# Kernel optimization log

Hardware: AMD Instinct MI355X
Metric: run time of the kernel (lower is better)

## Reference

```python
import jax, jax.numpy as jnp
import numpy as np

B, N, D, H, K = 8, 10000, 128, 4, 256
DH = D // H
M = N // 2


def make_pe(n, d):
    pos = jnp.arange(n, dtype=jnp.float32)[:, None]
    div = jnp.exp(jnp.arange(0, d, 2, dtype=jnp.float32) * (-jnp.log(10000.0) / d))
    ang = pos * div  # [n, d/2]
    pe = jnp.zeros((n, d), dtype=jnp.float32)
    pe = pe.at[:, 0::2].set(jnp.sin(ang))
    pe = pe.at[:, 1::2].set(jnp.cos(ang))
    return pe


def layernorm(z, g, b, eps=1e-5):
    mu = jnp.mean(z, -1, keepdims=True)
    var = jnp.var(z, -1, keepdims=True)
    return (z - mu) / jnp.sqrt(var + eps) * g + b


def setup_inputs():
    key = jax.random.key(0)
    ks = jax.random.split(key, 12)
    def rn(k, shape, scale):
        return jax.random.normal(k, shape, dtype=jnp.float32) * scale
    return {
        "x": rn(ks[0], (B, N), 1.0),
        "emb_w": rn(ks[1], (D, 1), 0.5),
        "emb_b": rn(ks[2], (D,), 0.02),
        "ln1_g": jnp.ones((D,), jnp.float32),
        "ln1_b": jnp.zeros((D,), jnp.float32),
        "wq": rn(ks[3], (D, D), D ** -0.5),
        "wk": rn(ks[4], (D, D), D ** -0.5),
        "wv": rn(ks[5], (D, D), D ** -0.5),
        "proj_k": rn(ks[6], (N, K), N ** -0.5),
        "proj_v": rn(ks[7], (N, K), N ** -0.5),
        "wo": rn(ks[8], (D, D), D ** -0.5),
        "wo_b": jnp.zeros((D,), jnp.float32),
        "ln2_g": jnp.ones((D,), jnp.float32),
        "ln2_b": jnp.zeros((D,), jnp.float32),
        "w1": rn(ks[9], (4 * D, D), D ** -0.5),
        "b1": jnp.zeros((4 * D,), jnp.float32),
        "w2": rn(ks[10], (D, 4 * D), (4 * D) ** -0.5),
        "b2": jnp.zeros((D,), jnp.float32),
        "fc_w": rn(ks[11], (M, N), N ** -0.5),
        "fc_b": jnp.zeros((M,), jnp.float32),
    }


def reference(x, emb_w, emb_b, ln1_g, ln1_b, wq, wk, wv, proj_k, proj_v, wo, wo_b,
              ln2_g, ln2_b, w1, b1, w2, b2, fc_w, fc_b):
    b, n = x.shape
    # Linear embedding of scalar per position: [B,N] -> [B,N,D]
    xe = x[..., None] @ emb_w.T + emb_b
    xe = xe + make_pe(n, D)
    # --- Linformer self-attention block (pre-norm + residual) ---
    hn = layernorm(xe, ln1_g, ln1_b)
    q = hn @ wq.T                                        # [B,N,D]
    k = jnp.einsum('bnd,nk->bkd', hn @ wk.T, proj_k)     # low-rank keys   [B,K,D]
    v = jnp.einsum('bnd,nk->bkd', hn @ wv.T, proj_v)     # low-rank values [B,K,D]
    q = q.reshape(b, n, H, DH).transpose(0, 2, 1, 3)     # [B,H,N,DH]
    k = k.reshape(b, K, H, DH).transpose(0, 2, 1, 3)     # [B,H,K,DH]
    v = v.reshape(b, K, H, DH).transpose(0, 2, 1, 3)
    attn = jax.nn.softmax(jnp.einsum('bhnd,bhkd->bhnk', q, k) * (DH ** -0.5), axis=-1)
    out = jnp.einsum('bhnk,bhkd->bhnd', attn, v).transpose(0, 2, 1, 3).reshape(b, n, D)
    xe = xe + out @ wo.T + wo_b
    # --- FeedForward block (pre-norm + residual, exact GELU) ---
    hn = layernorm(xe, ln2_g, ln2_b)
    xe = xe + (jax.nn.gelu(hn @ w1.T + b1, approximate=False) @ w2.T + b2)
    # fc over seq dim (Linear(N, N//2) applied to [B,D,N]) then sum-pool over D
    y = jnp.einsum('bnd,mn->bdm', xe, fc_w) + fc_b       # [B,D,M]
    return jnp.sum(y, axis=1)                            # [B,M]
```

## Files before the change

### kernel.cpp

```cpp
#include <hip/hip_runtime.h>

constexpr int B_ = 8, N_ = 10000, D_ = 128, H_ = 4, K_ = 256, M_ = 5000, DFF_ = 512;
constexpr int NPAD = 10240;

typedef __attribute__((ext_vector_type(8))) short bf16x8;
typedef __attribute__((ext_vector_type(4))) float f32x4;

__device__ __forceinline__ float bf2f(unsigned short u) {
    unsigned x = ((unsigned)u) << 16; float f; __builtin_memcpy(&f, &x, 4); return f;
}
__device__ __forceinline__ unsigned short f2bf(float f) {
    unsigned x; __builtin_memcpy(&x, &f, 4);
    x = (x + 0x7fffu + ((x >> 16) & 1u)) >> 16;
    return (unsigned short)x;
}
__device__ __forceinline__ unsigned pack2(float a, float b) {
    return (unsigned)f2bf(a) | ((unsigned)f2bf(b) << 16);
}
__device__ __forceinline__ float gelu_exact(float v) {
    return 0.5f * v * (1.0f + erff(v * 0.70710678118654752f));
}

__global__ __launch_bounds__(256) void cvt_w_k(
    const float* __restrict__ s0, const float* __restrict__ s1, const float* __restrict__ s2,
    const float* __restrict__ s3, const float* __restrict__ s4, const float* __restrict__ s5,
    unsigned short* __restrict__ d0, unsigned short* __restrict__ d1, unsigned short* __restrict__ d2,
    unsigned short* __restrict__ d3, unsigned short* __restrict__ d4, unsigned short* __restrict__ d5)
{
    const float* s; unsigned short* d; int sz;
    switch (blockIdx.y) {
        case 0: s = s0; d = d0; sz = 16384; break;
        case 1: s = s1; d = d1; sz = 16384; break;
        case 2: s = s2; d = d2; sz = 16384; break;
        case 3: s = s3; d = d3; sz = 16384; break;
        case 4: s = s4; d = d4; sz = 65536; break;
        default: s = s5; d = d5; sz = 65536; break;
    }
    const int idx = (blockIdx.x * 256 + threadIdx.x) * 8;
    if (idx >= sz) return;
    float4 a = *(const float4*)(s + idx);
    float4 b = *(const float4*)(s + idx + 4);
    uint4 p;
    p.x = pack2(a.x, a.y); p.y = pack2(a.z, a.w);
    p.z = pack2(b.x, b.y); p.w = pack2(b.z, b.w);
    *(uint4*)(d + idx) = p;
}

__global__ __launch_bounds__(256) void ptt_k(
    const float* __restrict__ pK, const float* __restrict__ pV, unsigned short* __restrict__ Pt)
{
    __shared__ __align__(16) char lds[16384];
    const int t = threadIdx.x;
    const int n0 = blockIdx.x * 64, k0 = blockIdx.y * 128, which = blockIdx.z;
    const float* P = which ? pV : pK;
    {
        const int nl = t >> 2, cc = t & 3;
        const int n = n0 + nl;
        uint4 v[4] = {};
        if (n < N_) {
            const float4* src = (const float4*)(P + (size_t)n * K_ + k0 + cc * 32);
            #pragma unroll
            for (int j = 0; j < 4; ++j) {
                float4 a = src[2 * j], b = src[2 * j + 1];
                uint4 p; p.x = pack2(a.x, a.y); p.y = pack2(a.z, a.w);
                p.z = pack2(b.x, b.y); p.w = pack2(b.z, b.w);
                v[j] = p;
            }
        }
        #pragma unroll
        for (int j = 0; j < 4; ++j) {
            int ch = (cc * 4 + j) ^ (nl & 15);
            *(uint4*)(lds + nl * 256 + ch * 16) = v[j];
        }
    }
    __syncthreads();
    {
        const int eb = t >> 3, nb = t & 7;
        unsigned short r0_[8], r1_[8], r2_[8], r3_[8];
        #pragma unroll
        for (int i = 0; i < 8; ++i) {
            int n = nb * 8 + i;
            int byte_ = n * 256 + (((eb >> 1) ^ (n & 15)) << 4) + ((eb & 1) << 3);
            uint2 dv = *(const uint2*)(lds + byte_);
            r0_[i] = (unsigned short)(dv.x & 0xffff); r1_[i] = (unsigned short)(dv.x >> 16);
            r2_[i] = (unsigned short)(dv.y & 0xffff); r3_[i] = (unsigned short)(dv.y >> 16);
        }
        size_t dbase = ((size_t)which * 256 + k0 + eb * 4) * NPAD + n0 + nb * 8;
        *(uint4*)&Pt[dbase]            = *(uint4*)r0_;
        *(uint4*)&Pt[dbase + NPAD]     = *(uint4*)r1_;
        *(uint4*)&Pt[dbase + 2 * NPAD] = *(uint4*)r2_;
        *(uint4*)&Pt[dbase + 3 * NPAD] = *(uint4*)r3_;
    }
}

__global__ __launch_bounds__(256) void hnt_k(
    const unsigned short* __restrict__ hn, unsigned short* __restrict__ hnT)
{
    __shared__ __align__(16) char lds[16384];
    const int t = threadIdx.x;
    const int n0 = blockIdx.x * 64, b = blockIdx.z;
    {
        const int nl = t >> 2, cc = t & 3;
        const int n = n0 + nl;
        uint4 v[4] = {};
        if (n < N_) {
            const uint4* src = (const uint4*)(hn + ((size_t)(b * N_ + n)) * D_ + cc * 32);
            #pragma unroll
            for (int j = 0; j < 4; ++j) v[j] = src[j];
        }
        #pragma unroll
        for (int j = 0; j < 4; ++j) {
            int ch = (cc * 4 + j) ^ (nl & 15);
            *(uint4*)(lds + nl * 256 + ch * 16) = v[j];
        }
    }
    __syncthreads();
    {
        const int eb = t >> 3, nb = t & 7;
        unsigned short r0_[8], r1_[8], r2_[8], r3_[8];
        #pragma unroll
        for (int i = 0; i < 8; ++i) {
            int n = nb * 8 + i;
            int byte_ = n * 256 + (((eb >> 1) ^ (n & 15)) << 4) + ((eb & 1) << 3);
            uint2 dv = *(const uint2*)(lds + byte_);
            r0_[i] = (unsigned short)(dv.x & 0xffff); r1_[i] = (unsigned short)(dv.x >> 16);
            r2_[i] = (unsigned short)(dv.y & 0xffff); r3_[i] = (unsigned short)(dv.y >> 16);
        }
        size_t dbase = ((size_t)b * 128 + eb * 4) * NPAD + n0 + nb * 8;
        *(uint4*)&hnT[dbase]            = *(uint4*)r0_;
        *(uint4*)&hnT[dbase + NPAD]     = *(uint4*)r1_;
        *(uint4*)&hnT[dbase + 2 * NPAD] = *(uint4*)r2_;
        *(uint4*)&hnT[dbase + 3 * NPAD] = *(uint4*)r3_;
    }
}

__global__ __launch_bounds__(256) void embed_ln_k(
    const float* __restrict__ x, const float* __restrict__ ew, const float* __restrict__ eb,
    const float* __restrict__ g, const float* __restrict__ bb,
    unsigned short* __restrict__ xeb, unsigned short* __restrict__ hnb)
{
    const int r = blockIdx.x * 4 + (threadIdx.x >> 6);
    const int lane = threadIdx.x & 63;
    const int n = r % N_;
    const float xv = x[r];
    const float ang = (float)n * expf((float)lane * -0.14391156829962788f);
    float sv, cv; sincosf(ang, &sv, &cv);
    const int d0 = 2 * lane;
    float e0 = xv * ew[d0]     + eb[d0]     + sv;
    float e1 = xv * ew[d0 + 1] + eb[d0 + 1] + cv;
    float sum = e0 + e1, sq = e0 * e0 + e1 * e1;
    #pragma unroll
    for (int off = 32; off; off >>= 1) { sum += __shfl_xor(sum, off); sq += __shfl_xor(sq, off); }
    const float mu = sum * (1.f / 128.f);
    const float var = sq * (1.f / 128.f) - mu * mu;
    const float rs = rsqrtf(var + 1e-5f);
    const size_t base = (size_t)r * D_ + d0;
    *(unsigned*)&xeb[base] = pack2(e0, e1);
    *(unsigned*)&hnb[base] = pack2((e0 - mu) * rs * g[d0] + bb[d0],
                                   (e1 - mu) * rs * g[d0 + 1] + bb[d0 + 1]);
}

enum { M_Q = 0, M_PROJ = 1, M_SMALL = 2, M_WO = 3, M_W1 = 4, M_W2 = 5 };

template<int MODE>
__global__ __launch_bounds__(256) void mgemm_k(
    const unsigned short* __restrict__ Abase, const unsigned short* __restrict__ Wbase,
    const unsigned short* __restrict__ Walt,
    const float* __restrict__ bias, float* __restrict__ Cf, unsigned short* __restrict__ Cb,
    const unsigned short* __restrict__ xebr, unsigned short* __restrict__ xebw,
    const float* __restrict__ lng, const float* __restrict__ lnb, float* __restrict__ st)
{
    constexpr int NSTEP = (MODE == M_PROJ) ? 40 : (MODE == M_W2 ? 16 : 4);
    constexpr int SA = (MODE == M_PROJ) ? NPAD : (MODE == M_W2 ? 512 : 128);
    constexpr int SB = SA;
    constexpr int NCTOT = (MODE == M_W1) ? 512 : 128;
    constexpr bool GELU = (MODE == M_W1);
    constexpr bool FUSED = (MODE == M_WO || MODE == M_W2);

    __shared__ __align__(16) char lds[16384];

    const int t = threadIdx.x;
    const int bx = blockIdx.x, by = blockIdx.y, bz = blockIdx.z;

    const unsigned short* Ag; const unsigned short* Wg; size_t cbase;
    if (MODE == M_PROJ) {
        const int b = (bz >> 3) & 7, chunk = bz & 7, which = bz >> 6;
        Ag = Abase + (size_t)which * 256 * NPAD + (size_t)bx * 128 * NPAD + chunk * 1280;
        Wg = Wbase + (size_t)b * 128 * NPAD + chunk * 1280;
        cbase = (size_t)bz * 32768 + (size_t)bx * 16384;
    } else if (MODE == M_SMALL) {
        Ag = Abase + (size_t)bz * 2048 * 128 + (size_t)bx * 128 * 128;
        Wg = bz ? Walt : Wbase;
        cbase = (size_t)bz * 262144 + (size_t)bx * 16384;
    } else {
        Ag = Abase + (size_t)bx * 128 * SA;
        Wg = Wbase + (size_t)by * 128 * SB;
        cbase = (size_t)bx * 128 * NCTOT + (size_t)by * 128;
    }

    const int srow = t >> 1, hib = 2 * (t & 1);
    const unsigned short* aptr = Ag + (size_t)srow * SA + hib * 8;
    const unsigned short* wptr = Wg + (size_t)srow * SB + hib * 8;
    const int swz = (srow >> 1) & 3;
    char* la0 = lds + srow * 64 + ((hib ^ swz) << 4);
    char* la1 = lds + srow * 64 + (((hib + 1) ^ swz) << 4);
    char* lw0 = la0 + 8192;
    char* lw1 = la1 + 8192;

    const int w = t >> 6, l = t & 63;
    const int g = l >> 4;
    const int wrow = (w & 1) * 64, wcol = (w >> 1) * 64;
    int offA[4], offW[4];
    #pragma unroll
    for (int mi = 0; mi < 4; ++mi) {
        int ra = wrow + mi * 16 + (l & 15);
        offA[mi] = ra * 64 + (((l >> 4) ^ ((ra >> 1) & 3)) << 4);
        int rw = wcol + mi * 16 + (l & 15);
        offW[mi] = 8192 + rw * 64 + (((l >> 4) ^ ((rw >> 1) & 3)) << 4);
    }

    f32x4 acc[4][4] = {};

    for (int s = 0; s < NSTEP; ++s) {
        uint4 va0 = *(const uint4*)(aptr);
        uint4 va1 = *(const uint4*)(aptr + 8);
        uint4 vw0 = *(const uint4*)(wptr);
        uint4 vw1 = *(const uint4*)(wptr + 8);
        aptr += 32; wptr += 32;
        __syncthreads();
        *(uint4*)la0 = va0; *(uint4*)la1 = va1;
        *(uint4*)lw0 = vw0; *(uint4*)lw1 = vw1;
        __syncthreads();
        bf16x8 af[4], bfr[4];
        #pragma unroll
        for (int mi = 0; mi < 4; ++mi) {
            af[mi] = *(const bf16x8*)(lds + offA[mi]);
            bfr[mi] = *(const bf16x8*)(lds + offW[mi]);
        }
        #pragma unroll
        for (int mi = 0; mi < 4; ++mi)
            #pragma unroll
            for (int ni = 0; ni < 4; ++ni)
                acc[mi][ni] = __builtin_amdgcn_mfma_f32_16x16x32_bf16(af[mi], bfr[ni], acc[mi][ni], 0, 0, 0);
    }

    const int lrb = wrow + (g << 2);
    const int lcb = wcol + (l & 15);

    if (FUSED) {
        float rsum[4][4], rsq[4][4];
        #pragma unroll
        for (int mi = 0; mi < 4; ++mi)
            #pragma unroll
            for (int r = 0; r < 4; ++r) { rsum[mi][r] = 0.f; rsq[mi][r] = 0.f; }
        #pragma unroll
        for (int mi = 0; mi < 4; ++mi)
            #pragma unroll
            for (int ni = 0; ni < 4; ++ni) {
                const int lc = lcb + ni * 16;
                #pragma unroll
                for (int r = 0; r < 4; ++r) {
                    const int lr = lrb + mi * 16 + r;
                    const size_t ci = cbase + (size_t)lr * 128 + lc;
                    float v = acc[mi][ni][r] + bias[lc] + bf2f(xebr[ci]);
                    acc[mi][ni][r] = v;
                    rsum[mi][r] += v;
                    if (MODE == M_WO) rsq[mi][r] += v * v;
                }
            }
        #pragma unroll
        for (int mi = 0; mi < 4; ++mi)
            #pragma unroll
            for (int r = 0; r < 4; ++r) {
                float s_ = rsum[mi][r], q_ = rsq[mi][r];
                #pragma unroll
                for (int off = 1; off < 16; off <<= 1) {
                    s_ += __shfl_xor(s_, off);
                    if (MODE == M_WO) q_ += __shfl_xor(q_, off);
                }
                rsum[mi][r] = s_; rsq[mi][r] = q_;
            }
        __syncthreads();
        float2* red = (float2*)lds;
        if ((l & 15) == 0) {
            #pragma unroll
            for (int mi = 0; mi < 4; ++mi)
                #pragma unroll
                for (int r = 0; r < 4; ++r) {
                    const int lr = lrb + mi * 16 + r;
                    float2 e; e.x = rsum[mi][r]; e.y = rsq[mi][r];
                    red[(w >> 1) * 128 + lr] = e;
                }
        }
        __syncthreads();
        if (MODE == M_WO) {
            #pragma unroll
            for (int mi = 0; mi < 4; ++mi)
                #pragma unroll
                for (int r = 0; r < 4; ++r) {
                    const int lr = lrb + mi * 16 + r;
                    const float2 e0 = red[lr], e1 = red[128 + lr];
                    const float mu = (e0.x + e1.x) * (1.f / 128.f);
                    const float var = (e0.y + e1.y) * (1.f / 128.f) - mu * mu;
                    const float rstd = rsqrtf(var + 1e-5f);
                    #pragma unroll
                    for (int ni = 0; ni < 4; ++ni) {
                        const int lc = lcb + ni * 16;
                        const size_t ci = cbase + (size_t)lr * 128 + lc;
                        const float xv = acc[mi][ni][r];
                        xebw[ci] = f2bf(xv);
                        Cb[ci] = f2bf((xv - mu) * rstd * lng[lc] + lnb[lc]);
                    }
                }
        } else {
            if ((l & 15) == 0 && (w >> 1) == 0) {
                #pragma unroll
                for (int mi = 0; mi < 4; ++mi)
                    #pragma unroll
                    for (int r = 0; r < 4; ++r) {
                        const int lr = lrb + mi * 16 + r;
                        const float total = red[lr].x + red[128 + lr].x;
                        const int grow = bx * 128 + lr;
                        const int bidx = grow / N_;
                        const int n = grow - bidx * N_;
                        st[(size_t)n * 8 + bidx] = total;
                    }
            }
        }
        return;
    }

    constexpr bool HASBIAS = (MODE == M_W1);
    constexpr bool OBF = (MODE == M_Q || MODE == M_W1 || MODE == M_SMALL);
    #pragma unroll
    for (int mi = 0; mi < 4; ++mi) {
        #pragma unroll
        for (int ni = 0; ni < 4; ++ni) {
            const int lc = lcb + ni * 16;
            #pragma unroll
            for (int r = 0; r < 4; ++r) {
                const int lr = lrb + mi * 16 + r;
                float v = acc[mi][ni][r];
                if (HASBIAS) v += bias[by * 128 + lc];
                if (GELU) v = gelu_exact(v);
                const size_t ci = cbase + (size_t)lr * NCTOT + lc;
                if (OBF) Cb[ci] = f2bf(v); else Cf[ci] = v;
            }
        }
    }
}

__global__ __launch_bounds__(256) void reduce_k(
    const float* __restrict__ partials, unsigned short* __restrict__ lowKV)
{
    const int gid = blockIdx.x * 256 + threadIdx.x;
    const int wb = gid >> 15, r = gid & 32767;
    const float* p = partials + (size_t)wb * 8 * 32768 + r;
    float s = 0.f;
    #pragma unroll
    for (int c = 0; c < 8; ++c) s += p[c * 32768];
    lowKV[gid] = f2bf(s);
}

__global__ __launch_bounds__(256) void attn_mfma_k(
    const unsigned short* __restrict__ q, const unsigned short* __restrict__ kv,
    unsigned short* __restrict__ outp)
{
    __shared__ __align__(16) char lds[65536];
    const int t = threadIdx.x;
    const int w = t >> 6, l = t & 63;
    const int g = l >> 4, ql = l & 15;
    const int h = blockIdx.y, b = blockIdx.z;
    const int q0 = blockIdx.x * 256;
    const float SC = 0.17677669529663687f;

    #pragma unroll
    for (int i = 0; i < 4; ++i) {
        const int r = (t >> 2) + 64 * i;
        const uint4 v = *(const uint4*)(kv + ((size_t)(b * 256 + r) * 128 + h * 32) + (t & 3) * 8);
        *(uint4*)(lds + r * 64 + (((t & 3) * 16) ^ ((r & 3) << 4))) = v;
    }
    {
        const int kp = t & 127, dhalf = t >> 7;
        const unsigned short* vsrc = kv + 262144 + ((size_t)(b * 256 + 2 * kp) * 128 + h * 32 + 16 * dhalf);
        uint4 a0 = *(const uint4*)(vsrc);
        uint4 a1 = *(const uint4*)(vsrc + 8);
        uint4 c0 = *(const uint4*)(vsrc + 128);
        uint4 c1 = *(const uint4*)(vsrc + 136);
        const unsigned short* pa0 = (const unsigned short*)&a0;
        const unsigned short* pa1 = (const unsigned short*)&a1;
        const unsigned short* pc0 = (const unsigned short*)&c0;
        const unsigned short* pc1 = (const unsigned short*)&c1;
        #pragma unroll
        for (int j = 0; j < 8; ++j) {
            const int row = 16 * dhalf + j;
            unsigned u = (unsigned)pa0[j] | ((unsigned)pc0[j] << 16);
            *(unsigned*)(lds + 16384 + row * 512 + ((4 * kp) ^ ((row & 7) << 4))) = u;
        }
        #pragma unroll
        for (int j = 0; j < 8; ++j) {
            const int row = 16 * dhalf + 8 + j;
            unsigned u = (unsigned)pa1[j] | ((unsigned)pc1[j] << 16);
            *(unsigned*)(lds + 16384 + row * 512 + ((4 * kp) ^ ((row & 7) << 4))) = u;
        }
    }
    bf16x8 qfr[4];
    #pragma unroll
    for (int qf = 0; qf < 4; ++qf) {
        int n = q0 + w * 64 + qf * 16 + ql;
        if (n >= N_) n = N_ - 1;
        qfr[qf] = *(const bf16x8*)(q + ((size_t)(b * N_ + n) * 128 + h * 32 + g * 8));
    }
    __syncthreads();

    char* Pw = lds + 32768 + w * 8192;
    f32x4 oacc[2][4] = {};
    float m_run[4], l_run[4];
    #pragma unroll
    for (int qf = 0; qf < 4; ++qf) { m_run[qf] = -1e30f; l_run[qf] = 0.f; }

    for (int kt = 0; kt < 4; ++kt) {
        const int kb = kt * 64;
        bf16x8 kfr[4];
        #pragma unroll
        for (int kf = 0; kf < 4; ++kf) {
            const int r = kb + kf * 16 + ql;
            kfr[kf] = *(const bf16x8*)(lds + r * 64 + ((g * 16) ^ ((r & 3) << 4)));
        }
        f32x4 s_[4][4];
        #pragma unroll
        for (int kf = 0; kf < 4; ++kf)
            #pragma unroll
            for (int qf = 0; qf < 4; ++qf) {
                f32x4 z = {0.f, 0.f, 0.f, 0.f};
                s_[kf][qf] = __builtin_amdgcn_mfma_f32_16x16x32_bf16(kfr[kf], qfr[qf], z, 0, 0, 0);
            }
        #pragma unroll
        for (int qf = 0; qf < 4; ++qf) {
            float mx = -1e30f;
            #pragma unroll
            for (int kf = 0; kf < 4; ++kf)
                #pragma unroll
                for (int r = 0; r < 4; ++r) mx = fmaxf(mx, s_[kf][qf][r]);
            mx = fmaxf(mx, __shfl_xor(mx, 16));
            mx = fmaxf(mx, __shfl_xor(mx, 32));
            mx *= SC;
            if (mx > m_run[qf]) {
                const float corr = __expf(m_run[qf] - mx);
                l_run[qf] *= corr;
                #pragma unroll
                for (int df = 0; df < 2; ++df) {
                    oacc[df][qf][0] *= corr; oacc[df][qf][1] *= corr;
                    oacc[df][qf][2] *= corr; oacc[df][qf][3] *= corr;
                }
                m_run[qf] = mx;
            }
            float p_[4][4]; float ssum = 0.f;
            #pragma unroll
            for (int kf = 0; kf < 4; ++kf)
                #pragma unroll
                for (int r = 0; r < 4; ++r) {
                    const float pv = __expf(s_[kf][qf][r] * SC - m_run[qf]);
                    p_[kf][r] = pv; ssum += pv;
                }
            ssum += __shfl_xor(ssum, 16);
            ssum += __shfl_xor(ssum, 32);
            l_run[qf] += ssum;
            const int qrow = qf * 16 + ql;
            #pragma unroll
            for (int kf = 0; kf < 4; ++kf) {
                uint2 pk;
                pk.x = pack2(p_[kf][0], p_[kf][1]);
                pk.y = pack2(p_[kf][2], p_[kf][3]);
                *(uint2*)(Pw + qrow * 128 + ((kf * 32 + g * 8) ^ ((qrow & 7) << 4))) = pk;
            }
        }
        asm volatile("s_waitcnt lgkmcnt(0)" ::: "memory");
        __builtin_amdgcn_sched_barrier(0);
        #pragma unroll
        for (int ks = 0; ks < 2; ++ks) {
            bf16x8 vt_[2];
            #pragma unroll
            for (int df = 0; df < 2; ++df) {
                const int row = df * 16 + ql;
                vt_[df] = *(const bf16x8*)(lds + 16384 + row * 512 +
                           ((kb * 2 + ks * 64 + g * 16) ^ ((row & 7) << 4)));
            }
            #pragma unroll
            for (int qf = 0; qf < 4; ++qf) {
                const int qrow = qf * 16 + ql;
                bf16x8 pf = *(const bf16x8*)(Pw + qrow * 128 + ((ks * 64 + g * 16) ^ ((qrow & 7) << 4)));
                #pragma unroll
                for (int df = 0; df < 2; ++df)
                    oacc[df][qf] = __builtin_amdgcn_mfma_f32_16x16x32_bf16(vt_[df], pf, oacc[df][qf], 0, 0, 0);
            }
        }
        asm volatile("s_waitcnt lgkmcnt(0)" ::: "memory");
        __builtin_amdgcn_sched_barrier(0);
    }

    float inv_[4];
    #pragma unroll
    for (int qf = 0; qf < 4; ++qf) inv_[qf] = 1.f / l_run[qf];
    #pragma unroll
    for (int qf = 0; qf < 4; ++qf) {
        const int qrow = qf * 16 + ql;
        #pragma unroll
        for (int df = 0; df < 2; ++df) {
            const unsigned lo = pack2(oacc[df][qf][0] * inv_[qf], oacc[df][qf][1] * inv_[qf]);
            const unsigned hi = pack2(oacc[df][qf][2] * inv_[qf], oacc[df][qf][3] * inv_[qf]);
            *(unsigned*)(Pw + qrow * 64 + ((df * 32 + g * 8) ^ ((qrow & 3) << 4))) = lo;
            *(unsigned*)(Pw + qrow * 64 + ((df * 32 + g * 8 + 4) ^ ((qrow & 3) << 4))) = hi;
        }
    }
    asm volatile("s_waitcnt lgkmcnt(0)" ::: "memory");
    __builtin_amdgcn_sched_barrier(0);
    #pragma unroll
    for (int pp = 0; pp < 4; ++pp) {
        const int qrow = pp * 16 + (l >> 2), c = l & 3;
        const uint4 v = *(const uint4*)(Pw + qrow * 64 + ((c * 16) ^ ((qrow & 3) << 4)));
        const int n = q0 + w * 64 + qrow;
        if (n < N_)
            *(uint4*)(outp + ((size_t)(b * N_ + n) * 128 + h * 32 + c * 8)) = v;
    }
}

__global__ __launch_bounds__(256) void fc_k(
    const float* __restrict__ st, const float* __restrict__ fcw, const float* __restrict__ fcb,
    float* __restrict__ out)
{
    __shared__ float wred[4][4][8];
    const int t = threadIdx.x;
    const int m0 = blockIdx.x * 4;
    float acc[4][8] = {};
    for (int n = t; n < N_; n += 256) {
        const float4 sa = *(const float4*)&st[(size_t)n * 8];
        const float4 sb = *(const float4*)&st[(size_t)n * 8 + 4];
        #pragma unroll
        for (int mm = 0; mm < 4; ++mm) {
            const float w = fcw[(size_t)(m0 + mm) * N_ + n];
            acc[mm][0] = fmaf(w, sa.x, acc[mm][0]); acc[mm][1] = fmaf(w, sa.y, acc[mm][1]);
            acc[mm][2] = fmaf(w, sa.z, acc[mm][2]); acc[mm][3] = fmaf(w, sa.w, acc[mm][3]);
            acc[mm][4] = fmaf(w, sb.x, acc[mm][4]); acc[mm][5] = fmaf(w, sb.y, acc[mm][5]);
            acc[mm][6] = fmaf(w, sb.z, acc[mm][6]); acc[mm][7] = fmaf(w, sb.w, acc[mm][7]);
        }
    }
    #pragma unroll
    for (int mm = 0; mm < 4; ++mm)
        #pragma unroll
        for (int bb = 0; bb < 8; ++bb) {
            float v = acc[mm][bb];
            #pragma unroll
            for (int off = 32; off; off >>= 1) v += __shfl_xor(v, off);
            acc[mm][bb] = v;
        }
    const int lane = t & 63, wv_ = t >> 6;
    if (lane == 0)
        #pragma unroll
        for (int mm = 0; mm < 4; ++mm)
            #pragma unroll
            for (int bb = 0; bb < 8; ++bb) wred[wv_][mm][bb] = acc[mm][bb];
    __syncthreads();
    if (t < 32) {
        const int mm = t >> 3, bb = t & 7;
        float v = wred[0][mm][bb] + wred[1][mm][bb] + wred[2][mm][bb] + wred[3][mm][bb];
        out[(size_t)bb * M_ + m0 + mm] = v + 128.f * fcb[m0 + mm];
    }
}

extern "C" void kernel_launch(void* const* d_in, const int* in_sizes, int n_in,
                              void* d_out, int out_size, void* d_ws, size_t ws_size,
                              hipStream_t stream)
{
    const float* x      = (const float*)d_in[0];
    const float* emb_w  = (const float*)d_in[1];
    const float* emb_b  = (const float*)d_in[2];
    const float* ln1_g  = (const float*)d_in[3];
    const float* ln1_b  = (const float*)d_in[4];
    const float* wq     = (const float*)d_in[5];
    const float* wk     = (const float*)d_in[6];
    const float* wv     = (const float*)d_in[7];
    const float* projk  = (const float*)d_in[8];
    const float* projv  = (const float*)d_in[9];
    const float* wo     = (const float*)d_in[10];
    const float* wo_b   = (const float*)d_in[11];
    const float* ln2_g  = (const float*)d_in[12];
    const float* ln2_b  = (const float*)d_in[13];
    const float* w1     = (const float*)d_in[14];
    const float* b1     = (const float*)d_in[15];
    const float* w2     = (const float*)d_in[16];
    const float* b2     = (const float*)d_in[17];
    const float* fcw    = (const float*)d_in[18];
    const float* fcb    = (const float*)d_in[19];
    float* out = (float*)d_out;

    char* W = (char*)d_ws;
    unsigned short* xeb      = (unsigned short*)W;
    unsigned short* hnb      = (unsigned short*)(W + 40960000);
    char*           region   = W + 61440000;
    unsigned short* qb       = (unsigned short*)region;
    unsigned short* hnT      = (unsigned short*)(region + 20480000);
    unsigned short* Pt       = (unsigned short*)(region + 41451520);
    float*          partials = (float*)(region + 51937280);
    unsigned short* hid      = (unsigned short*)region;
    unsigned short* lowKV    = (unsigned short*)(W + 146931712);
    unsigned short* klowb    = (unsigned short*)(W + 147980288);
    unsigned short* wqb      = (unsigned short*)(W + 150077440);
    unsigned short* wkb      = wqb + 16384;
    unsigned short* wvb      = wkb + 16384;
    unsigned short* wob      = wvb + 16384;
    unsigned short* w1b      = wob + 16384;
    unsigned short* w2b      = w1b + 65536;
    float*          st       = (float*)(W + 150470656);

    const size_t BN = (size_t)B_ * N_;

    cvt_w_k<<<dim3(32, 6), 256, 0, stream>>>(wq, wk, wv, wo, w1, w2, wqb, wkb, wvb, wob, w1b, w2b);
    ptt_k<<<dim3(160, 2, 2), 256, 0, stream>>>(projk, projv, Pt);
    embed_ln_k<<<BN / 4, 256, 0, stream>>>(x, emb_w, emb_b, ln1_g, ln1_b, xeb, hnb);
    hnt_k<<<dim3(160, 1, 8), 256, 0, stream>>>(hnb, hnT);
    mgemm_k<M_Q><<<dim3(625, 1, 1), 256, 0, stream>>>(hnb, wqb, nullptr, nullptr, nullptr, qb,
                                                      nullptr, nullptr, nullptr, nullptr, nullptr);
    mgemm_k<M_PROJ><<<dim3(2, 1, 128), 256, 0, stream>>>(Pt, hnT, nullptr, nullptr, partials, nullptr,
                                                         nullptr, nullptr, nullptr, nullptr, nullptr);
    reduce_k<<<2048, 256, 0, stream>>>(partials, lowKV);
    mgemm_k<M_SMALL><<<dim3(16, 1, 2), 256, 0, stream>>>(lowKV, wkb, wvb, nullptr, nullptr, klowb,
                                                         nullptr, nullptr, nullptr, nullptr, nullptr);
    attn_mfma_k<<<dim3(40, H_, B_), 256, 0, stream>>>(qb, klowb, hnb);
    mgemm_k<M_WO><<<dim3(625, 1, 1), 256, 0, stream>>>(hnb, wob, nullptr, wo_b, nullptr, hnb,
                                                       xeb, xeb, ln2_g, ln2_b, nullptr);
    mgemm_k<M_W1><<<dim3(625, 4, 1), 256, 0, stream>>>(hnb, w1b, nullptr, b1, nullptr, hid,
                                                       nullptr, nullptr, nullptr, nullptr, nullptr);
    mgemm_k<M_W2><<<dim3(625, 1, 1), 256, 0, stream>>>(hid, w2b, nullptr, b2, nullptr, nullptr,
                                                       xeb, nullptr, nullptr, nullptr, st);
    fc_k<<<M_ / 4, 256, 0, stream>>>(st, fcw, fcb, out);
}
```

Baseline: 328.8 us.

## Fuse FFN into one kernel, merge prep kernels, fold reduction into GEMM

Replaces the separate W1 (with GELU) and W2 GEMM launches with a single fused FFN kernel. The 512-wide hidden activation now stays in shared memory per 64-row tile instead of going through a global buffer. The two prep kernels are merged into one launch, and the partial-sum reduction for the low-rank K/V is folded into the small GEMM's A-load. The fc kernel is also vectorized to load four positions at a time. The FFN kernel reads weight fragments directly from global memory without LDS staging, and its smaller tiles may cost some MFMA efficiency.

```diff
diff --git a/kernel.cpp b/kernel.cpp
--- a/kernel.cpp
+++ b/kernel.cpp
@@ -21,37 +21,42 @@
     return 0.5f * v * (1.0f + erff(v * 0.70710678118654752f));
 }
 
-__global__ __launch_bounds__(256) void cvt_w_k(
-    const float* __restrict__ s0, const float* __restrict__ s1, const float* __restrict__ s2,
-    const float* __restrict__ s3, const float* __restrict__ s4, const float* __restrict__ s5,
-    unsigned short* __restrict__ d0, unsigned short* __restrict__ d1, unsigned short* __restrict__ d2,
-    unsigned short* __restrict__ d3, unsigned short* __restrict__ d4, unsigned short* __restrict__ d5)
-{
-    const float* s; unsigned short* d; int sz;
-    switch (blockIdx.y) {
-        case 0: s = s0; d = d0; sz = 16384; break;
-        case 1: s = s1; d = d1; sz = 16384; break;
-        case 2: s = s2; d = d2; sz = 16384; break;
-        case 3: s = s3; d = d3; sz = 16384; break;
-        case 4: s = s4; d = d4; sz = 65536; break;
-        default: s = s5; d = d5; sz = 65536; break;
-    }
-    const int idx = (blockIdx.x * 256 + threadIdx.x) * 8;
-    if (idx >= sz) return;
-    float4 a = *(const float4*)(s + idx);
-    float4 b = *(const float4*)(s + idx + 4);
-    uint4 p;
-    p.x = pack2(a.x, a.y); p.y = pack2(a.z, a.w);
-    p.z = pack2(b.x, b.y); p.w = pack2(b.z, b.w);
-    *(uint4*)(d + idx) = p;
-}
-
-__global__ __launch_bounds__(256) void ptt_k(
+__global__ __launch_bounds__(256) void prep_k(
+    const float* __restrict__ wq, const float* __restrict__ wk, const float* __restrict__ wv,
+    const float* __restrict__ wo, const float* __restrict__ w1, const float* __restrict__ w2,
+    unsigned short* __restrict__ wqb, unsigned short* __restrict__ wkb, unsigned short* __restrict__ wvb,
+    unsigned short* __restrict__ wob, unsigned short* __restrict__ w1b, unsigned short* __restrict__ w2b,
     const float* __restrict__ pK, const float* __restrict__ pV, unsigned short* __restrict__ Pt)
 {
     __shared__ __align__(16) char lds[16384];
     const int t = threadIdx.x;
-    const int n0 = blockIdx.x * 64, k0 = blockIdx.y * 128, which = blockIdx.z;
+    const int flat = blockIdx.x;
+
+    if (flat < 192) {
+        const int by = flat / 32, bx = flat % 32;
+        const float* s; unsigned short* d; int sz;
+        switch (by) {
+            case 0: s = wq; d = wqb; sz = 16384; break;
+            case 1: s = wk; d = wkb; sz = 16384; break;
+            case 2: s = wv; d = wvb; sz = 16384; break;
+            case 3: s = wo; d = wob; sz = 16384; break;
+            case 4: s = w1; d = w1b; sz = 65536; break;
+            default: s = w2; d = w2b; sz = 65536; break;
+        }
+        const int idx = (bx * 256 + t) * 8;
+        if (idx >= sz) return;
+        float4 a = *(const float4*)(s + idx);
+        float4 b = *(const float4*)(s + idx + 4);
+        uint4 p;
+        p.x = pack2(a.x, a.y); p.y = pack2(a.z, a.w);
+        p.z = pack2(b.x, b.y); p.w = pack2(b.z, b.w);
+        *(uint4*)(d + idx) = p;
+        return;
+    }
+
+    const int f = flat - 192;
+    const int bx = f % 160, rest = f / 160;
+    const int n0 = bx * 64, k0 = (rest & 1) * 128, which = rest >> 1;
     const float* P = which ? pV : pK;
     {
         const int nl = t >> 2, cc = t & 3;
@@ -160,7 +165,7 @@
                                    (e1 - mu) * rs * g[d0 + 1] + bb[d0 + 1]);
 }
 
-enum { M_Q = 0, M_PROJ = 1, M_SMALL = 2, M_WO = 3, M_W1 = 4, M_W2 = 5 };
+enum { M_Q = 0, M_PROJ = 1, M_SMALL = 2, M_WO = 3 };
 
 template<int MODE>
 __global__ __launch_bounds__(256) void mgemm_k(
@@ -168,38 +173,35 @@
     const unsigned short* __restrict__ Walt,
     const float* __restrict__ bias, float* __restrict__ Cf, unsigned short* __restrict__ Cb,
     const unsigned short* __restrict__ xebr, unsigned short* __restrict__ xebw,
-    const float* __restrict__ lng, const float* __restrict__ lnb, float* __restrict__ st)
+    const float* __restrict__ lng, const float* __restrict__ lnb)
 {
-    constexpr int NSTEP = (MODE == M_PROJ) ? 40 : (MODE == M_W2 ? 16 : 4);
-    constexpr int SA = (MODE == M_PROJ) ? NPAD : (MODE == M_W2 ? 512 : 128);
+    constexpr int NSTEP = (MODE == M_PROJ) ? 40 : 4;
+    constexpr int SA = (MODE == M_PROJ) ? NPAD : 128;
     constexpr int SB = SA;
-    constexpr int NCTOT = (MODE == M_W1) ? 512 : 128;
-    constexpr bool GELU = (MODE == M_W1);
-    constexpr bool FUSED = (MODE == M_WO || MODE == M_W2);
+    constexpr bool FUSED = (MODE == M_WO);
 
     __shared__ __align__(16) char lds[16384];
 
     const int t = threadIdx.x;
-    const int bx = blockIdx.x, by = blockIdx.y, bz = blockIdx.z;
-
-    const unsigned short* Ag; const unsigned short* Wg; size_t cbase;
+    const int bx = blockIdx.x, bz = blockIdx.z;
+
+    const unsigned short* Ag = nullptr; const unsigned short* Wg; size_t cbase;
     if (MODE == M_PROJ) {
         const int b = (bz >> 3) & 7, chunk = bz & 7, which = bz >> 6;
         Ag = Abase + (size_t)which * 256 * NPAD + (size_t)bx * 128 * NPAD + chunk * 1280;
         Wg = Wbase + (size_t)b * 128 * NPAD + chunk * 1280;
         cbase = (size_t)bz * 32768 + (size_t)bx * 16384;
     } else if (MODE == M_SMALL) {
-        Ag = Abase + (size_t)bz * 2048 * 128 + (size_t)bx * 128 * 128;
         Wg = bz ? Walt : Wbase;
         cbase = (size_t)bz * 262144 + (size_t)bx * 16384;
     } else {
         Ag = Abase + (size_t)bx * 128 * SA;
-        Wg = Wbase + (size_t)by * 128 * SB;
-        cbase = (size_t)bx * 128 * NCTOT + (size_t)by * 128;
+        Wg = Wbase;
+        cbase = (size_t)bx * 128 * 128;
     }
 
     const int srow = t >> 1, hib = 2 * (t & 1);
-    const unsigned short* aptr = Ag + (size_t)srow * SA + hib * 8;
+    const unsigned short* aptr = (MODE == M_SMALL) ? nullptr : Ag + (size_t)srow * SA + hib * 8;
     const unsigned short* wptr = Wg + (size_t)srow * SB + hib * 8;
     const int swz = (srow >> 1) & 3;
     char* la0 = lds + srow * 64 + ((hib ^ swz) << 4);
@@ -222,11 +224,37 @@
     f32x4 acc[4][4] = {};
 
     for (int s = 0; s < NSTEP; ++s) {
-        uint4 va0 = *(const uint4*)(aptr);
-        uint4 va1 = *(const uint4*)(aptr + 8);
+        uint4 va0, va1;
+        if (MODE == M_SMALL) {
+            const float* pb = Cf + (size_t)(bz * 8 + (bx >> 1)) * 262144
+                            + (bx & 1) * 16384 + (size_t)srow * 128 + s * 32 + hib * 8;
+            float a16[16];
+            #pragma unroll
+            for (int j = 0; j < 16; ++j) a16[j] = 0.f;
+            #pragma unroll
+            for (int c = 0; c < 8; ++c) {
+                const float* pc = pb + c * 32768;
+                const float4 f0 = *(const float4*)(pc);
+                const float4 f1 = *(const float4*)(pc + 4);
+                const float4 f2 = *(const float4*)(pc + 8);
+                const float4 f3 = *(const float4*)(pc + 12);
+                a16[0] += f0.x;  a16[1] += f0.y;  a16[2] += f0.z;  a16[3] += f0.w;
+                a16[4] += f1.x;  a16[5] += f1.y;  a16[6] += f1.z;  a16[7] += f1.w;
+                a16[8] += f2.x;  a16[9] += f2.y;  a16[10] += f2.z; a16[11] += f2.w;
+                a16[12] += f3.x; a16[13] += f3.y; a16[14] += f3.z; a16[15] += f3.w;
+            }
+            va0.x = pack2(a16[0], a16[1]);   va0.y = pack2(a16[2], a16[3]);
+            va0.z = pack2(a16[4], a16[5]);   va0.w = pack2(a16[6], a16[7]);
+            va1.x = pack2(a16[8], a16[9]);   va1.y = pack2(a16[10], a16[11]);
+            va1.z = pack2(a16[12], a16[13]); va1.w = pack2(a16[14], a16[15]);
+        } else {
+            va0 = *(const uint4*)(aptr);
+            va1 = *(const uint4*)(aptr + 8);
+            aptr += 32;
+        }
         uint4 vw0 = *(const uint4*)(wptr);
         uint4 vw1 = *(const uint4*)(wptr + 8);
-        aptr += 32; wptr += 32;
+        wptr += 32;
         __syncthreads();
         *(uint4*)la0 = va0; *(uint4*)la1 = va1;
         *(uint4*)lw0 = vw0; *(uint4*)lw1 = vw1;
@@ -265,7 +293,7 @@
                     float v = acc[mi][ni][r] + bias[lc] + bf2f(xebr[ci]);
                     acc[mi][ni][r] = v;
                     rsum[mi][r] += v;
-                    if (MODE == M_WO) rsq[mi][r] += v * v;
+                    rsq[mi][r] += v * v;
                 }
             }
         #pragma unroll
@@ -276,7 +304,7 @@
                 #pragma unroll
                 for (int off = 1; off < 16; off <<= 1) {
                     s_ += __shfl_xor(s_, off);
-                    if (MODE == M_WO) q_ += __shfl_xor(q_, off);
+                    q_ += __shfl_xor(q_, off);
                 }
                 rsum[mi][r] = s_; rsq[mi][r] = q_;
             }
@@ -293,45 +321,28 @@
                 }
         }
         __syncthreads();
-        if (MODE == M_WO) {
-            #pragma unroll
-            for (int mi = 0; mi < 4; ++mi)
-                #pragma unroll
-                for (int r = 0; r < 4; ++r) {
-                    const int lr = lrb + mi * 16 + r;
-                    const float2 e0 = red[lr], e1 = red[128 + lr];
-                    const float mu = (e0.x + e1.x) * (1.f / 128.f);
-                    const float var = (e0.y + e1.y) * (1.f / 128.f) - mu * mu;
-                    const float rstd = rsqrtf(var + 1e-5f);
-                    #pragma unroll
-                    for (int ni = 0; ni < 4; ++ni) {
-                        const int lc = lcb + ni * 16;
-                        const size_t ci = cbase + (size_t)lr * 128 + lc;
-                        const float xv = acc[mi][ni][r];
-                        xebw[ci] = f2bf(xv);
-                        Cb[ci] = f2bf((xv - mu) * rstd * lng[lc] + lnb[lc]);
-                    }
+        #pragma unroll
+        for (int mi = 0; mi < 4; ++mi)
+            #pragma unroll
+            for (int r = 0; r < 4; ++r) {
+                const int lr = lrb + mi * 16 + r;
+                const float2 e0 = red[lr], e1 = red[128 + lr];
+                const float mu = (e0.x + e1.x) * (1.f / 128.f);
+                const float var = (e0.y + e1.y) * (1.f / 128.f) - mu * mu;
+                const float rstd = rsqrtf(var + 1e-5f);
+                #pragma unroll
+                for (int ni = 0; ni < 4; ++ni) {
+                    const int lc = lcb + ni * 16;
+                    const size_t ci = cbase + (size_t)lr * 128 + lc;
+                    const float xv = acc[mi][ni][r];
+                    xebw[ci] = f2bf(xv);
+                    Cb[ci] = f2bf((xv - mu) * rstd * lng[lc] + lnb[lc]);
                 }
-        } else {
-            if ((l & 15) == 0 && (w >> 1) == 0) {
-                #pragma unroll
-                for (int mi = 0; mi < 4; ++mi)
-                    #pragma unroll
-                    for (int r = 0; r < 4; ++r) {
-                        const int lr = lrb + mi * 16 + r;
-                        const float total = red[lr].x + red[128 + lr].x;
-                        const int grow = bx * 128 + lr;
-                        const int bidx = grow / N_;
-                        const int n = grow - bidx * N_;
-                        st[(size_t)n * 8 + bidx] = total;
-                    }
-            }
-        }
+            }
         return;
     }
 
-    constexpr bool HASBIAS = (MODE == M_W1);
-    constexpr bool OBF = (MODE == M_Q || MODE == M_W1 || MODE == M_SMALL);
+    constexpr bool OBF = (MODE == M_Q || MODE == M_SMALL);
     #pragma unroll
     for (int mi = 0; mi < 4; ++mi) {
         #pragma unroll
@@ -340,26 +351,144 @@
             #pragma unroll
             for (int r = 0; r < 4; ++r) {
                 const int lr = lrb + mi * 16 + r;
-                float v = acc[mi][ni][r];
-                if (HASBIAS) v += bias[by * 128 + lc];
-                if (GELU) v = gelu_exact(v);
-                const size_t ci = cbase + (size_t)lr * NCTOT + lc;
+                const float v = acc[mi][ni][r];
+                const size_t ci = cbase + (size_t)lr * 128 + lc;
                 if (OBF) Cb[ci] = f2bf(v); else Cf[ci] = v;
             }
         }
     }
 }
 
-__global__ __launch_bounds__(256) void reduce_k(
-    const float* __restrict__ partials, unsigned short* __restrict__ lowKV)
+__global__ __launch_bounds__(256) void ffn_k(
+    const unsigned short* __restrict__ hnb, const unsigned short* __restrict__ w1b,
+    const unsigned short* __restrict__ w2b, const float* __restrict__ b1,
+    const float* __restrict__ b2, const unsigned short* __restrict__ xeb,
+    float* __restrict__ st)
 {
-    const int gid = blockIdx.x * 256 + threadIdx.x;
-    const int wb = gid >> 15, r = gid & 32767;
-    const float* p = partials + (size_t)wb * 8 * 32768 + r;
-    float s = 0.f;
-    #pragma unroll
-    for (int c = 0; c < 8; ++c) s += p[c * 32768];
-    lowKV[gid] = f2bf(s);
+    __shared__ __align__(16) char lds[32768];
+    const int t = threadIdx.x;
+    const int w = t >> 6, l = t & 63;
+    const int g = l >> 4, ql = l & 15;
+    const int r0 = blockIdx.x * 64;
+    const int wrow = (w & 1) * 32, wcol = (w >> 1) * 64;
+    char* Ald = lds;
+    char* Hld = lds + 16384;
+
+    {
+        const int rr = t >> 2, cc = t & 3;
+        #pragma unroll
+        for (int j = 0; j < 4; ++j) {
+            const int ch = cc * 4 + j;
+            const uint4 v = *(const uint4*)(hnb + (size_t)(r0 + rr) * 128 + ch * 8);
+            *(uint4*)(Ald + rr * 256 + ((ch ^ (rr & 15)) << 4)) = v;
+        }
+    }
+    __syncthreads();
+
+    f32x4 acc[2][4] = {};
+    #pragma unroll
+    for (int hc = 0; hc < 4; ++hc) {
+        f32x4 hacc[2][4] = {};
+        #pragma unroll
+        for (int ks = 0; ks < 4; ++ks) {
+            const int e0 = ks * 32 + g * 8;
+            bf16x8 af[2], bf1[4];
+            #pragma unroll
+            for (int mi = 0; mi < 2; ++mi) {
+                const int row = wrow + mi * 16 + ql;
+                af[mi] = *(const bf16x8*)(Ald + row * 256 + (((e0 >> 3) ^ (row & 15)) << 4));
+            }
+            #pragma unroll
+            for (int ni = 0; ni < 4; ++ni) {
+                const int c = hc * 128 + wcol + ni * 16 + ql;
+                bf1[ni] = *(const bf16x8*)(w1b + (size_t)c * 128 + e0);
+            }
+            #pragma unroll
+            for (int mi = 0; mi < 2; ++mi)
+                #pragma unroll
+                for (int ni = 0; ni < 4; ++ni)
+                    hacc[mi][ni] = __builtin_amdgcn_mfma_f32_16x16x32_bf16(af[mi], bf1[ni], hacc[mi][ni], 0, 0, 0);
+        }
+        #pragma unroll
+        for (int mi = 0; mi < 2; ++mi)
+            #pragma unroll
+            for (int ni = 0; ni < 4; ++ni) {
+                const int col = wcol + ni * 16 + ql;
+                const float bias = b1[hc * 128 + col];
+                #pragma unroll
+                for (int r = 0; r < 4; ++r) {
+                    const int row = wrow + mi * 16 + g * 4 + r;
+                    const float hv = gelu_exact(hacc[mi][ni][r] + bias);
+                    *(unsigned short*)(Hld + row * 256 + (((col >> 3) ^ (row & 15)) << 4) + (col & 7) * 2) = f2bf(hv);
+                }
+            }
+        __syncthreads();
+        #pragma unroll
+        for (int ks = 0; ks < 4; ++ks) {
+            const int e0 = ks * 32 + g * 8;
+            bf16x8 ah[2], bf2_[4];
+            #pragma unroll
+            for (int mi = 0; mi < 2; ++mi) {
+                const int row = wrow + mi * 16 + ql;
+                ah[mi] = *(const bf16x8*)(Hld + row * 256 + (((e0 >> 3) ^ (row & 15)) << 4));
+            }
+            #pragma unroll
+            for (int ni = 0; ni < 4; ++ni) {
+                const int c = wcol + ni * 16 + ql;
+                bf2_[ni] = *(const bf16x8*)(w2b + (size_t)c * 512 + hc * 128 + e0);
+            }
+            #pragma unroll
+            for (int mi = 0; mi < 2; ++mi)
+                #pragma unroll
+                for (int ni = 0; ni < 4; ++ni)
+                    acc[mi][ni] = __builtin_amdgcn_mfma_f32_16x16x32_bf16(ah[mi], bf2_[ni], acc[mi][ni], 0, 0, 0);
+        }
+        __syncthreads();
+    }
+
+    float rsum[2][4];
+    #pragma unroll
+    for (int mi = 0; mi < 2; ++mi)
+        #pragma unroll
+        for (int r = 0; r < 4; ++r) rsum[mi][r] = 0.f;
+    #pragma unroll
+    for (int mi = 0; mi < 2; ++mi)
+        #pragma unroll
+        for (int ni = 0; ni < 4; ++ni) {
+            const int col = wcol + ni * 16 + ql;
+            const float bias = b2[col];
+            #pragma unroll
+            for (int r = 0; r < 4; ++r) {
+                const int row = wrow + mi * 16 + g * 4 + r;
+                const size_t ci = (size_t)(r0 + row) * 128 + col;
+                rsum[mi][r] += acc[mi][ni][r] + bias + bf2f(xeb[ci]);
+            }
+        }
+    #pragma unroll
+    for (int mi = 0; mi < 2; ++mi)
+        #pragma unroll
+        for (int r = 0; r < 4; ++r) {
+            float s_ = rsum[mi][r];
+            #pragma unroll
+            for (int off = 1; off < 16; off <<= 1) s_ += __shfl_xor(s_, off);
+            rsum[mi][r] = s_;
+        }
+    float* red = (float*)lds;
+    if (ql == 0) {
+        #pragma unroll
+        for (int mi = 0; mi < 2; ++mi)
+            #pragma unroll
+            for (int r = 0; r < 4; ++r)
+                red[(w >> 1) * 64 + wrow + mi * 16 + g * 4 + r] = rsum[mi][r];
+    }
+    __syncthreads();
+    if (t < 64) {
+        const float total = red[t] + red[64 + t];
+        const int grow = r0 + t;
+        const int bidx = grow / N_;
+        const int n = grow - bidx * N_;
+        st[(size_t)n * 8 + bidx] = total;
+    }
 }
 
 __global__ __launch_bounds__(256) void attn_mfma_k(
@@ -533,16 +662,23 @@
     const int t = threadIdx.x;
     const int m0 = blockIdx.x * 4;
     float acc[4][8] = {};
-    for (int n = t; n < N_; n += 256) {
-        const float4 sa = *(const float4*)&st[(size_t)n * 8];
-        const float4 sb = *(const float4*)&st[(size_t)n * 8 + 4];
+    for (int n0 = t * 4; n0 < N_; n0 += 1024) {
+        float4 s_[8];
+        const float4* sp = (const float4*)&st[(size_t)n0 * 8];
+        #pragma unroll
+        for (int j = 0; j < 8; ++j) s_[j] = sp[j];
         #pragma unroll
         for (int mm = 0; mm < 4; ++mm) {
-            const float w = fcw[(size_t)(m0 + mm) * N_ + n];
-            acc[mm][0] = fmaf(w, sa.x, acc[mm][0]); acc[mm][1] = fmaf(w, sa.y, acc[mm][1]);
-            acc[mm][2] = fmaf(w, sa.z, acc[mm][2]); acc[mm][3] = fmaf(w, sa.w, acc[mm][3]);
-            acc[mm][4] = fmaf(w, sb.x, acc[mm][4]); acc[mm][5] = fmaf(w, sb.y, acc[mm][5]);
-            acc[mm][6] = fmaf(w, sb.z, acc[mm][6]); acc[mm][7] = fmaf(w, sb.w, acc[mm][7]);
+            const float4 wv4 = *(const float4*)&fcw[(size_t)(m0 + mm) * N_ + n0];
+            const float wv_[4] = {wv4.x, wv4.y, wv4.z, wv4.w};
+            #pragma unroll
+            for (int nn = 0; nn < 4; ++nn) {
+                const float4 sa = s_[nn * 2], sb = s_[nn * 2 + 1];
+                acc[mm][0] = fmaf(wv_[nn], sa.x, acc[mm][0]); acc[mm][1] = fmaf(wv_[nn], sa.y, acc[mm][1]);
+                acc[mm][2] = fmaf(wv_[nn], sa.z, acc[mm][2]); acc[mm][3] = fmaf(wv_[nn], sa.w, acc[mm][3]);
+                acc[mm][4] = fmaf(wv_[nn], sb.x, acc[mm][4]); acc[mm][5] = fmaf(wv_[nn], sb.y, acc[mm][5]);
+                acc[mm][6] = fmaf(wv_[nn], sb.z, acc[mm][6]); acc[mm][7] = fmaf(wv_[nn], sb.w, acc[mm][7]);
+            }
         }
     }
     #pragma unroll
@@ -602,8 +738,6 @@
     unsigned short* hnT      = (unsigned short*)(region + 20480000);
     unsigned short* Pt       = (unsigned short*)(region + 41451520);
     float*          partials = (float*)(region + 51937280);
-    unsigned short* hid      = (unsigned short*)region;
-    unsigned short* lowKV    = (unsigned short*)(W + 146931712);
     unsigned short* klowb    = (unsigned short*)(W + 147980288);
     unsigned short* wqb      = (unsigned short*)(W + 150077440);
     unsigned short* wkb      = wqb + 16384;
@@ -615,23 +749,19 @@
 
     const size_t BN = (size_t)B_ * N_;
 
-    cvt_w_k<<<dim3(32, 6), 256, 0, stream>>>(wq, wk, wv, wo, w1, w2, wqb, wkb, wvb, wob, w1b, w2b);
-    ptt_k<<<dim3(160, 2, 2), 256, 0, stream>>>(projk, projv, Pt);
+    prep_k<<<832, 256, 0, stream>>>(wq, wk, wv, wo, w1, w2, wqb, wkb, wvb, wob, w1b, w2b,
+                                    projk, projv, Pt);
     embed_ln_k<<<BN / 4, 256, 0, stream>>>(x, emb_w, emb_b, ln1_g, ln1_b, xeb, hnb);
     hnt_k<<<dim3(160, 1, 8), 256, 0, stream>>>(hnb, hnT);
     mgemm_k<M_Q><<<dim3(625, 1, 1), 256, 0, stream>>>(hnb, wqb, nullptr, nullptr, nullptr, qb,
-                                                      nullptr, nullptr, nullptr, nullptr, nullptr);
+                                                      nullptr, nullptr, nullptr, nullptr);
     mgemm_k<M_PROJ><<<dim3(2, 1, 128), 256, 0, stream>>>(Pt, hnT, nullptr, nullptr, partials, nullptr,
-                                                         nullptr, nullptr, nullptr, nullptr, nullptr);
-    reduce_k<<<2048, 256, 0, stream>>>(partials, lowKV);
-    mgemm_k<M_SMALL><<<dim3(16, 1, 2), 256, 0, stream>>>(lowKV, wkb, wvb, nullptr, nullptr, klowb,
-                                                         nullptr, nullptr, nullptr, nullptr, nullptr);
+                                                         nullptr, nullptr, nullptr, nullptr);
+    mgemm_k<M_SMALL><<<dim3(16, 1, 2), 256, 0, stream>>>(nullptr, wkb, wvb, nullptr, partials, klowb,
+                                                         nullptr, nullptr, nullptr, nullptr);
     attn_mfma_k<<<dim3(40, H_, B_), 256, 0, stream>>>(qb, klowb, hnb);
     mgemm_k<M_WO><<<dim3(625, 1, 1), 256, 0, stream>>>(hnb, wob, nullptr, wo_b, nullptr, hnb,
-                                                       xeb, xeb, ln2_g, ln2_b, nullptr);
-    mgemm_k<M_W1><<<dim3(625, 4, 1), 256, 0, stream>>>(hnb, w1b, nullptr, b1, nullptr, hid,
-                                                       nullptr, nullptr, nullptr, nullptr, nullptr);
-    mgemm_k<M_W2><<<dim3(625, 1, 1), 256, 0, stream>>>(hid, w2b, nullptr, b2, nullptr, nullptr,
-                                                       xeb, nullptr, nullptr, nullptr, st);
+                                                       xeb, xeb, ln2_g, ln2_b);
+    ffn_k<<<1250, 256, 0, stream>>>(hnb, w1b, w2b, b1, b2, xeb, st);
     fc_k<<<M_ / 4, 256, 0, stream>>>(st, fcw, fcb, out);
 }
```

Result: slower. 386.4 us (+17.5%).
